# Performance work log

Hardware: AMD Instinct MI355X
Metric: run time of the kernel (lower is better)

## Reference

```python
import jax, jax.numpy as jnp
import numpy as np

B, S, H = 2, 2048, 1024
NQ, NKV, HD, RANK = 16, 4, 64, 8
THETA = 10000.0
LORA_SCALE = 16 / RANK  # alpha / rank = 2.0
ATTN_SCALE = 1.0 / np.sqrt(HD)


def setup_inputs() -> dict:
    key = jax.random.key(0)
    ks = jax.random.split(key, 14)
    n = lambda k, shape, s: jax.random.normal(k, shape, jnp.float32) * s
    return {
        "x": n(ks[0], (B, S, H), 1.0),
        # nn.Linear weights: [out_features, in_features], y = x @ W.T (scaled small for stability)
        "Wq": n(ks[1], (NQ * HD, H), 0.02),
        "Wk": n(ks[2], (NKV * HD, H), 0.02),
        "Wv": n(ks[3], (NKV * HD, H), 0.02),
        "Wo": n(ks[4], (H, NQ * HD), 0.02),
        "qA": n(ks[5], (RANK, H), 0.05), "qB": n(ks[6], (NQ * HD, RANK), 0.05),
        "kA": n(ks[7], (RANK, H), 0.05), "kB": n(ks[8], (NKV * HD, RANK), 0.05),
        "vA": n(ks[9], (RANK, H), 0.05), "vB": n(ks[10], (NKV * HD, RANK), 0.05),
        "oA": n(ks[11], (RANK, NQ * HD), 0.05), "oB": n(ks[12], (H, RANK), 0.05),
    }


def _lora_proj(x, W, A, Bm):
    # x @ W.T + ((x @ A.T) @ B.T) * lora_scaling
    return x @ W.T + ((x @ A.T) @ Bm.T) * LORA_SCALE


def _rope(x, cos_h, sin_h):
    # x: [b, h, s, d]; even/odd interleaved split, concatenated output (matches torch ref)
    x1, x2 = x[..., ::2], x[..., 1::2]
    return jnp.concatenate([x1 * cos_h - x2 * sin_h, x1 * sin_h + x2 * cos_h], axis=-1)


def _forward(x, Wq, Wk, Wv, Wo, qA, qB, kA, kB, vA, vB, oA, oB):
    b, s, _ = x.shape
    q = _lora_proj(x, Wq, qA, qB).reshape(b, s, NQ, HD).transpose(0, 2, 1, 3)
    k = _lora_proj(x, Wk, kA, kB).reshape(b, s, NKV, HD).transpose(0, 2, 1, 3)
    v = _lora_proj(x, Wv, vA, vB).reshape(b, s, NKV, HD).transpose(0, 2, 1, 3)

    inv_freq = 1.0 / (THETA ** (jnp.arange(0, HD, 2, dtype=jnp.float32) / HD))  # [HD/2]
    freqs = jnp.arange(s, dtype=jnp.float32)[:, None] * inv_freq[None, :]  # [s, HD/2]
    cos_h = jnp.cos(freqs)[None, None]  # [1,1,s,HD/2]
    sin_h = jnp.sin(freqs)[None, None]
    q = _rope(q, cos_h, sin_h)
    k = _rope(k, cos_h, sin_h)

    rep = NQ // NKV  # GQA: repeat_interleave along head axis
    k = jnp.repeat(k, rep, axis=1)
    v = jnp.repeat(v, rep, axis=1)

    attn = jax.nn.softmax(jnp.einsum('bhqd,bhkd->bhqk', q, k) * ATTN_SCALE, axis=-1)
    out = jnp.einsum('bhqk,bhkd->bhqd', attn, v)
    out = out.transpose(0, 2, 1, 3).reshape(b, s, NQ * HD)
    return _lora_proj(out, Wo, oA, oB)


def reference(x, Wq, Wk, Wv, Wo, qA, qB, kA, kB, vA, vB, oA, oB):
    return _forward(x, Wq, Wk, Wv, Wo, qA, qB, kA, kB, vA, vB, oA, oB)
```

## Files before the change

### kernel.cpp

```cpp
#include <hip/hip_runtime.h>

typedef _Float16 f16;
typedef __attribute__((ext_vector_type(8))) _Float16 f16x8;
typedef __attribute__((ext_vector_type(4))) float f32x4;

#define DI __device__ __forceinline__
#define MFMA16(a, b, c) __builtin_amdgcn_mfma_f32_16x16x32_f16(a, b, c, 0, 0, 0)

constexpr int BB = 2, SS = 2048, HH = 1024;
constexpr int NQ = 16, NKV = 4, HD = 64;
constexpr int NTOK = BB * SS;
constexpr int NQKV = NQ*HD + 2*NKV*HD;

DI f32x4 zero4() { f32x4 z = {0.f, 0.f, 0.f, 0.f}; return z; }

DI float fexp2(float x) {
#if __has_builtin(__builtin_amdgcn_exp2f)
  return __builtin_amdgcn_exp2f(x);
#else
  return exp2f(x);
#endif
}

DI unsigned pk2(float a, float b) {
#if __has_builtin(__builtin_amdgcn_cvt_pkrtz)
  typedef __fp16 fp16v2 __attribute__((ext_vector_type(2)));
  union { fp16v2 h; unsigned u; } c;
  c.h = __builtin_amdgcn_cvt_pkrtz(a, b);
  return c.u;
#else
  union { f16 h[2]; unsigned u; } c;
  c.h[0] = (f16)a; c.h[1] = (f16)b; return c.u;
#endif
}

DI void glds16(const void* g, void* l) {
  __builtin_amdgcn_global_load_lds((const __attribute__((address_space(1))) void*)g,
                                   (__attribute__((address_space(3))) void*)l, 16, 0, 0);
}

DI int shuf32(int i) {
  return (i & ~31) | (((i >> 2) & 3) << 3) | (i & 3) | (((i >> 4) & 1) << 2);
}

__global__ __launch_bounds__(256) void prep_kernel(
    const float* __restrict__ x,
    const float* __restrict__ Wq, const float* __restrict__ Wk,
    const float* __restrict__ Wv, const float* __restrict__ Wo,
    const float* __restrict__ qA, const float* __restrict__ qB,
    const float* __restrict__ kA, const float* __restrict__ kB,
    const float* __restrict__ vA, const float* __restrict__ vB,
    const float* __restrict__ oA, const float* __restrict__ oB,
    f16* __restrict__ xh, f16* __restrict__ Wqkv, f16* __restrict__ Woe,
    float* __restrict__ ctab, float* __restrict__ stab) {
  int idx = blockIdx.x * 256 + threadIdx.x;
  if (idx < NQKV * HH) {
    int n = idx >> 10, hcol = idx & 1023;
    const float *Am, *Bm; float wv; int nn;
    if (n < 1024)      { nn = n;        wv = Wq[idx];              Am = qA; Bm = qB; }
    else if (n < 1280) { nn = n - 1024; wv = Wk[nn*1024 + hcol];   Am = kA; Bm = kB; }
    else               { nn = n - 1280; wv = Wv[nn*1024 + hcol];   Am = vA; Bm = vB; }
    float s = 0.f;
#pragma unroll
    for (int r = 0; r < 8; ++r) s += Bm[nn*8 + r] * Am[r*1024 + hcol];
    Wqkv[shuf32(idx)] = (f16)(wv + 2.0f * s);
  } else if ((idx -= NQKV * HH) < 1024 * 1024) {
    int n = idx >> 10, hcol = idx & 1023;
    float s = 0.f;
#pragma unroll
    for (int r = 0; r < 8; ++r) s += oB[n*8 + r] * oA[r*1024 + hcol];
    Woe[shuf32(idx)] = (f16)(Wo[idx] + 2.0f * s);
  } else if ((idx -= 1024 * 1024) < NTOK * HH) {
    xh[shuf32(idx)] = (f16)x[idx];
  } else if ((idx -= NTOK * HH) < SS * 32) {
    int s = idx >> 5, d = idx & 31;
    float inv = expf(-(float)d * 0.28782313662425583f);
    float ang = (float)s * inv;
    ctab[idx] = cosf(ang);
    stab[idx] = sinf(ang);
  }
}

template<typename OUT_T>
__global__ __launch_bounds__(256, 2) void gemm_bt(const f16* __restrict__ A, const f16* __restrict__ Bw,
                                                  OUT_T* __restrict__ C, int M, int N, int K) {
  __shared__ char lds[65536];
  const int nt = N >> 7;
  const int nwg = (M >> 7) * nt;
  int bid = blockIdx.x;
  const int cpx = nwg >> 3;
  bid = (bid & 7) * cpx + (bid >> 3);
  const int m0 = (bid / nt) << 7;
  const int n0 = (bid % nt) << 7;
  const int tid = threadIdx.x;
  const int lane = tid & 63;
  const int w = tid >> 6, wr = w >> 1, wc = w & 1;
  const int l15 = lane & 15, g = (lane >> 4) & 3;
  const char* Ab = (const char*)A;
  const char* Bb = (const char*)Bw;
  const size_t Kb = (size_t)K * 2;
  const int srow = tid >> 3;
  const int scol = (tid & 7) << 4;

  auto stage = [&](int kt, int bs) {
    char* ab = lds + bs * 32768;
    char* bbuf = ab + 16384;
    const size_t kbyte = (size_t)kt << 7;
#pragma unroll
    for (int s = 0; s < 4; ++s) {
      int row = (s << 5) + srow;
      glds16(Ab + (size_t)(m0 + row) * Kb + kbyte + (scol ^ ((row & 7) << 4)),
             ab + (s << 12) + (w << 10));
    }
#pragma unroll
    for (int s = 0; s < 4; ++s) {
      int row = (s << 5) + srow;
      glds16(Bb + (size_t)(n0 + row) * Kb + kbyte + (scol ^ ((row & 7) << 4)),
             bbuf + (s << 12) + (w << 10));
    }
  };

  f32x4 acc[4][4];
#pragma unroll
  for (int i = 0; i < 4; ++i)
#pragma unroll
    for (int j = 0; j < 4; ++j) acc[i][j] = zero4();

  const int nkt = K >> 6;
  stage(0, 0);
  for (int t = 0; t < nkt; ++t) {
    __syncthreads();
    if (t + 1 < nkt) stage(t + 1, (t + 1) & 1);
    const char* ab = lds + (t & 1) * 32768;
    const char* bbuf = ab + 16384;
    f16x8 af[4][2], bf[4][2];
#pragma unroll
    for (int mi = 0; mi < 4; ++mi) {
      int ra = (wr << 6) + (mi << 4) + l15;
      int base = ra << 7, sw = (ra & 7) << 4;
#pragma unroll
      for (int kk = 0; kk < 2; ++kk)
        af[mi][kk] = *reinterpret_cast<const f16x8*>(ab + base + ((((kk << 6) + (g << 4))) ^ sw));
    }
#pragma unroll
    for (int nj = 0; nj < 4; ++nj) {
      int rb = (wc << 6) + (nj << 4) + l15;
      int base = rb << 7, sw = (rb & 7) << 4;
#pragma unroll
      for (int kk = 0; kk < 2; ++kk)
        bf[nj][kk] = *reinterpret_cast<const f16x8*>(bbuf + base + ((((kk << 6) + (g << 4))) ^ sw));
    }
#pragma unroll
    for (int mi = 0; mi < 4; ++mi)
#pragma unroll
      for (int nj = 0; nj < 4; ++nj) {
        acc[mi][nj] = MFMA16(af[mi][0], bf[nj][0], acc[mi][nj]);
        acc[mi][nj] = MFMA16(af[mi][1], bf[nj][1], acc[mi][nj]);
      }
  }
#pragma unroll
  for (int mi = 0; mi < 4; ++mi)
#pragma unroll
    for (int nj = 0; nj < 4; ++nj) {
      int mmb = m0 + (wr << 6) + (mi << 4) + (g << 2);
      int nn  = n0 + (wc << 6) + (nj << 4) + l15;
      f32x4 a = acc[mi][nj];
#pragma unroll
      for (int r = 0; r < 4; ++r) C[(size_t)(mmb + r) * N + nn] = (OUT_T)a[r];
    }
}

__global__ __launch_bounds__(256) void rope_kernel(const f16* __restrict__ qkv,
    const float* __restrict__ ctab, const float* __restrict__ stab,
    f16* __restrict__ Qr, f16* __restrict__ Kr) {
  int idx = blockIdx.x * 256 + threadIdx.x;
  int dp = idx & 31;
  int t = idx >> 5;
  int hh = t % 20;
  int tok = t / 20;
  int s = tok & (SS - 1), b = tok >> 11;
  float c  = ctab[(s << 5) + dp];
  float sn = stab[(s << 5) + dp];
  const f16* row = qkv + (size_t)tok * NQKV;
  int p1 = (((dp >> 2) & 3) << 3) | (dp & 3) | (((dp >> 4) & 1) << 2);
  if (hh < 16) {
    float x1 = (float)row[hh*64 + 2*dp], x2 = (float)row[hh*64 + 2*dp + 1];
    f16* out = Qr + ((size_t)(b*NQ + hh)*SS + s) * HD;
    constexpr float QS = 0.18033688011112042f;
    out[p1]      = (f16)(QS * (x1*c  - x2*sn));
    out[p1 + 32] = (f16)(QS * (x1*sn + x2*c));
  } else {
    int hk = hh - 16;
    float x1 = (float)row[1024 + hk*64 + 2*dp], x2 = (float)row[1024 + hk*64 + 2*dp + 1];
    f16* out = Kr + ((size_t)(b*NKV + hk)*SS + s) * HD;
    out[p1]      = (f16)(x1*c  - x2*sn);
    out[p1 + 32] = (f16)(x1*sn + x2*c);
  }
}

__global__ __launch_bounds__(256) void vtrans_kernel(const f16* __restrict__ qkv,
                                                     f16* __restrict__ Vt) {
  __shared__ f16 Ls[64 * 72];
  const int tid = threadIdx.x;
  const int blk = blockIdx.x;
  const int st = blk & 31, hkv = (blk >> 5) & 3, b = blk >> 7;
  const int s0 = st << 6;
  {
    int s = tid >> 2, d0 = (tid & 3) << 4;
    const f16* src = qkv + ((size_t)(b*SS + s0 + s)) * NQKV + 1280 + hkv*64 + d0;
    uint4 v0 = *reinterpret_cast<const uint4*>(src);
    uint4 v1 = *reinterpret_cast<const uint4*>(src + 8);
    *reinterpret_cast<uint4*>(Ls + s * 72 + d0) = v0;
    *reinterpret_cast<uint4*>(Ls + s * 72 + d0 + 8) = v1;
  }
  __syncthreads();
  int d = tid >> 2;
  f16* dst = Vt + ((size_t)(b*NKV + hkv)*64 + d) * SS + s0;
#pragma unroll
  for (int cc = 0; cc < 2; ++cc) {
    int cch = ((tid & 3) << 1) + cc;
    int m = cch >> 2, g = cch & 3;
    union { f16 h[8]; uint4 u; } o;
#pragma unroll
    for (int j = 0; j < 8; ++j) {
      int sl = (m << 5) + (g << 2) + (j & 3) + ((j >> 2) << 4);
      o.h[j] = Ls[sl * 72 + d];
    }
    *reinterpret_cast<uint4*>(dst + (cch << 3)) = o.u;
  }
}

__global__ __launch_bounds__(512, 4) void attn_kernel(
    const f16* __restrict__ Qr, const f16* __restrict__ Kr,
    const f16* __restrict__ Vt, f16* __restrict__ AO) {
  __shared__ char lds[3 * 16384];
  const int tid = threadIdx.x, lane = tid & 63, w = tid >> 6;
  const int l15 = lane & 15, g = (lane >> 4) & 3;
  const int bh = blockIdx.x;
  const int b = bh >> 4, h = bh & 15, hkv = h >> 2;
  const int q0 = blockIdx.y << 8;
  const char* Kbase = (const char*)(Kr + (size_t)(b*NKV + hkv) * SS * HD);
  const char* Vbase = (const char*)(Vt + (size_t)(b*NKV + hkv) * HD * SS);

  f16x8 qf[2][2];
  {
    const f16* qr0 = Qr + ((size_t)(b*NQ + h)*SS + q0 + (w << 5) + l15) * HD + (g << 3);
    qf[0][0] = *reinterpret_cast<const f16x8*>(qr0);
    qf[0][1] = *reinterpret_cast<const f16x8*>(qr0 + 32);
    qf[1][0] = *reinterpret_cast<const f16x8*>(qr0 + 16*HD);
    qf[1][1] = *reinterpret_cast<const f16x8*>(qr0 + 16*HD + 32);
  }
  f16x8 ones;
#pragma unroll
  for (int i = 0; i < 8; ++i) ones[i] = (f16)1.0f;
  const f32x4 minit = {-4.f, -4.f, -4.f, -4.f};

  f32x4 acc[4][2];
#pragma unroll
  for (int i = 0; i < 4; ++i) { acc[i][0] = zero4(); acc[i][1] = zero4(); }
  f32x4 es0 = zero4(), es1 = zero4();

  const int srow = tid >> 3;
  const int scolb = (tid & 7) << 4;
  auto stage = [&](int kv0, int buf) {
    char* kb = lds + buf * 16384;
    char* vb = kb + 8192;
    glds16(Kbase + (size_t)(kv0 + srow) * 128 + (scolb ^ ((srow & 7) << 4)),
           kb + (w << 10));
    glds16(Vbase + (size_t)srow * 4096 + (kv0 << 1) + (scolb ^ ((srow & 7) << 4)),
           vb + (w << 10));
  };

  stage(0, 0);
  stage(64, 1);
  int cur = 0;

  for (int t = 0; t < 32; ++t) {
    if (t < 31) asm volatile("s_waitcnt vmcnt(2)" ::: "memory");
    else        asm volatile("s_waitcnt vmcnt(0)" ::: "memory");
    __builtin_amdgcn_s_barrier();
    __builtin_amdgcn_sched_barrier(0);
    int nb = cur + 2; if (nb >= 3) nb -= 3;
    if (t + 2 < 32) stage((t + 2) << 6, nb);

    const char* kb = lds + cur * 16384;
    const char* vb = kb + 8192;

    f32x4 sf0[4], sf1[4];
    __builtin_amdgcn_s_setprio(1);
#pragma unroll
    for (int mb = 0; mb < 4; ++mb) {
      int rowK = (mb << 4) + l15;
      int Bk = (rowK << 7) + ((g << 4) ^ ((rowK & 7) << 4));
      f16x8 kf0 = *reinterpret_cast<const f16x8*>(kb + Bk);
      f16x8 kf1 = *reinterpret_cast<const f16x8*>(kb + (Bk ^ 64));
      f32x4 z0 = minit, z1 = minit;
      z0 = MFMA16(kf0, qf[0][0], z0); z0 = MFMA16(kf1, qf[0][1], z0);
      z1 = MFMA16(kf0, qf[1][0], z1); z1 = MFMA16(kf1, qf[1][1], z1);
      sf0[mb] = z0; sf1[mb] = z1;
    }
    __builtin_amdgcn_s_setprio(0);

    union { unsigned u[8]; f16x8 v[2]; } p0, p1;
#pragma unroll
    for (int j = 0; j < 8; ++j) {
      int mb = j >> 1, r0 = (j & 1) << 1;
      p0.u[j] = pk2(fexp2(sf0[mb][r0]), fexp2(sf0[mb][r0 + 1]));
      p1.u[j] = pk2(fexp2(sf1[mb][r0]), fexp2(sf1[mb][r0 + 1]));
    }

    __builtin_amdgcn_s_setprio(1);
#pragma unroll
    for (int sh = 0; sh < 2; ++sh) {
#pragma unroll
      for (int db = 0; db < 4; ++db) {
        int rowV = (db << 4) + l15;
        int Bv = (rowV << 7) + ((g << 4) ^ ((rowV & 7) << 4));
        f16x8 vf = *reinterpret_cast<const f16x8*>(vb + (Bv ^ (sh << 6)));
        acc[db][0] = MFMA16(vf, p0.v[sh], acc[db][0]);
        acc[db][1] = MFMA16(vf, p1.v[sh], acc[db][1]);
      }
      es0 = MFMA16(ones, p0.v[sh], es0);
      es1 = MFMA16(ones, p1.v[sh], es1);
    }
    __builtin_amdgcn_s_setprio(0);

    cur += 1; if (cur == 3) cur = 0;
  }

  float i0 = 1.0f / es0[0], i1 = 1.0f / es1[0];
  int sg0 = q0 + (w << 5) + l15;
  size_t ob0 = ((size_t)b * SS + sg0) * 1024 + h * 64;
  size_t ob1 = ob0 + (size_t)16 * 1024;
#pragma unroll
  for (int db = 0; db < 4; ++db) {
    union { f16 hv[4]; uint2 u; } o0, o1;
#pragma unroll
    for (int r = 0; r < 4; ++r) {
      o0.hv[r] = (f16)(acc[db][0][r] * i0);
      o1.hv[r] = (f16)(acc[db][1][r] * i1);
    }
    int pos = ((db >> 1) << 5) + (g << 3) + ((db & 1) << 2);
    *reinterpret_cast<uint2*>(AO + ob0 + pos) = o0.u;
    *reinterpret_cast<uint2*>(AO + ob1 + pos) = o1.u;
  }
}

extern "C" void kernel_launch(void* const* d_in, const int* in_sizes, int n_in,
                              void* d_out, int out_size, void* d_ws, size_t ws_size,
                              hipStream_t stream) {
  const float* x  = (const float*)d_in[0];
  const float* Wq = (const float*)d_in[1];
  const float* Wk = (const float*)d_in[2];
  const float* Wv = (const float*)d_in[3];
  const float* Wo = (const float*)d_in[4];
  const float* qA = (const float*)d_in[5];
  const float* qB = (const float*)d_in[6];
  const float* kA = (const float*)d_in[7];
  const float* kB = (const float*)d_in[8];
  const float* vA = (const float*)d_in[9];
  const float* vB = (const float*)d_in[10];
  const float* oA = (const float*)d_in[11];
  const float* oB = (const float*)d_in[12];
  char* ws = (char*)d_ws;
  f16* xh    = (f16*)(ws);
  f16* Wqkv  = (f16*)(ws + 8388608);
  f16* Woe   = (f16*)(ws + 11534336);
  f16* qkv   = (f16*)(ws + 13631488);
  f16* Qr    = (f16*)(ws + 26214400);
  f16* Kr    = (f16*)(ws + 34603008);
  f16* Vt    = (f16*)(ws + 36700160);
  float* ctab = (float*)(ws + 38797312);
  float* stab = (float*)(ws + 39059456);
  f16* AO = xh;
  float* out = (float*)d_out;

  prep_kernel<<<26880, 256, 0, stream>>>(x, Wq, Wk, Wv, Wo, qA, qB, kA, kB, vA, vB, oA, oB,
                                         xh, Wqkv, Woe, ctab, stab);
  gemm_bt<f16><<<dim3(32 * 12), 256, 0, stream>>>(xh, Wqkv, qkv, 4096, 1536, 1024);
  rope_kernel<<<10240, 256, 0, stream>>>(qkv, ctab, stab, Qr, Kr);
  vtrans_kernel<<<256, 256, 0, stream>>>(qkv, Vt);
  attn_kernel<<<dim3(32, 8), 512, 0, stream>>>(Qr, Kr, Vt, AO);
  gemm_bt<float><<<dim3(32 * 8), 256, 0, stream>>>(AO, Woe, out, 4096, 1024, 1024);
}
```

Before: 93.96 us.

## Split attention over two KV halves and add a combine kernel

The attention kernel now launches a third grid dimension of two splits, each covering half of the key/value sequence. Each split writes unnormalized f16 accumulators plus its row sums to workspace, and a new combine kernel adds the two partials and normalizes them. Because the softmax uses a fixed offset rather than a running max, the partials can simply be summed. The aim is to double the number of attention blocks so more of the GPU's compute units are busy; the cost is an extra launch, more memory traffic for the partials, and a risk of f16 overflow or precision loss in the unnormalized accumulators.

```diff
diff --git a/kernel.cpp b/kernel.cpp
--- a/kernel.cpp
+++ b/kernel.cpp
@@ -232,13 +232,16 @@
 
 __global__ __launch_bounds__(512, 4) void attn_kernel(
     const f16* __restrict__ Qr, const f16* __restrict__ Kr,
-    const f16* __restrict__ Vt, f16* __restrict__ AO) {
+    const f16* __restrict__ Vt, f16* __restrict__ pacc0,
+    f16* __restrict__ pacc1, float* __restrict__ pes) {
   __shared__ char lds[3 * 16384];
   const int tid = threadIdx.x, lane = tid & 63, w = tid >> 6;
   const int l15 = lane & 15, g = (lane >> 4) & 3;
   const int bh = blockIdx.x;
   const int b = bh >> 4, h = bh & 15, hkv = h >> 2;
   const int q0 = blockIdx.y << 8;
+  const int split = blockIdx.z;
+  const int kvbase = split << 10;
   const char* Kbase = (const char*)(Kr + (size_t)(b*NKV + hkv) * SS * HD);
   const char* Vbase = (const char*)(Vt + (size_t)(b*NKV + hkv) * HD * SS);
 
@@ -271,17 +274,18 @@
            vb + (w << 10));
   };
 
-  stage(0, 0);
-  stage(64, 1);
+  constexpr int NT = 16;
+  stage(kvbase, 0);
+  stage(kvbase + 64, 1);
   int cur = 0;
 
-  for (int t = 0; t < 32; ++t) {
-    if (t < 31) asm volatile("s_waitcnt vmcnt(2)" ::: "memory");
-    else        asm volatile("s_waitcnt vmcnt(0)" ::: "memory");
+  for (int t = 0; t < NT; ++t) {
+    if (t < NT - 1) asm volatile("s_waitcnt vmcnt(2)" ::: "memory");
+    else            asm volatile("s_waitcnt vmcnt(0)" ::: "memory");
     __builtin_amdgcn_s_barrier();
     __builtin_amdgcn_sched_barrier(0);
     int nb = cur + 2; if (nb >= 3) nb -= 3;
-    if (t + 2 < 32) stage((t + 2) << 6, nb);
+    if (t + 2 < NT) stage(kvbase + ((t + 2) << 6), nb);
 
     const char* kb = lds + cur * 16384;
     const char* vb = kb + 8192;
@@ -328,7 +332,7 @@
     cur += 1; if (cur == 3) cur = 0;
   }
 
-  float i0 = 1.0f / es0[0], i1 = 1.0f / es1[0];
+  f16* pout = split ? pacc1 : pacc0;
   int sg0 = q0 + (w << 5) + l15;
   size_t ob0 = ((size_t)b * SS + sg0) * 1024 + h * 64;
   size_t ob1 = ob0 + (size_t)16 * 1024;
@@ -337,13 +341,40 @@
     union { f16 hv[4]; uint2 u; } o0, o1;
 #pragma unroll
     for (int r = 0; r < 4; ++r) {
-      o0.hv[r] = (f16)(acc[db][0][r] * i0);
-      o1.hv[r] = (f16)(acc[db][1][r] * i1);
+      o0.hv[r] = (f16)acc[db][0][r];
+      o1.hv[r] = (f16)acc[db][1][r];
     }
     int pos = ((db >> 1) << 5) + (g << 3) + ((db & 1) << 2);
-    *reinterpret_cast<uint2*>(AO + ob0 + pos) = o0.u;
-    *reinterpret_cast<uint2*>(AO + ob1 + pos) = o1.u;
-  }
+    *reinterpret_cast<uint2*>(pout + ob0 + pos) = o0.u;
+    *reinterpret_cast<uint2*>(pout + ob1 + pos) = o1.u;
+  }
+  if (lane < 16) {
+    int qv = q0 + (w << 5) + lane;
+    float* pe = pes + ((size_t)(split*BB + b)*NQ + h)*SS;
+    pe[qv] = es0[0];
+    pe[qv + 16] = es1[0];
+  }
+}
+
+__global__ __launch_bounds__(256) void combine_kernel(
+    const f16* __restrict__ pacc0, const f16* __restrict__ pacc1,
+    const float* __restrict__ pes, f16* __restrict__ AO) {
+  int idx = blockIdx.x * 256 + threadIdx.x;
+  int e = idx << 3;
+  int tok = e >> 10;
+  int col = e & 1023;
+  int h = col >> 6;
+  int b = tok >> 11, q = tok & (SS - 1);
+  float e0 = pes[((size_t)(b)*NQ + h)*SS + q];
+  float e1 = pes[((size_t)(BB + b)*NQ + h)*SS + q];
+  float inv = 1.0f / (e0 + e1);
+  union { uint4 u; f16 h8[8]; } a, c, o;
+  a.u = *reinterpret_cast<const uint4*>(pacc0 + e);
+  c.u = *reinterpret_cast<const uint4*>(pacc1 + e);
+#pragma unroll
+  for (int j = 0; j < 8; ++j)
+    o.h8[j] = (f16)(((float)a.h8[j] + (float)c.h8[j]) * inv);
+  *reinterpret_cast<uint4*>(AO + e) = o.u;
 }
 
 extern "C" void kernel_launch(void* const* d_in, const int* in_sizes, int n_in,
@@ -372,7 +403,10 @@
   f16* Vt    = (f16*)(ws + 36700160);
   float* ctab = (float*)(ws + 38797312);
   float* stab = (float*)(ws + 39059456);
-  f16* AO = xh;
+  f16* pacc0 = xh;
+  f16* pacc1 = qkv;
+  float* pes = (float*)(ws + 13631488 + 8388608);
+  f16* AO = Qr;
   float* out = (float*)d_out;
 
   prep_kernel<<<26880, 256, 0, stream>>>(x, Wq, Wk, Wv, Wo, qA, qB, kA, kB, vA, vB, oA, oB,
@@ -380,6 +414,7 @@
   gemm_bt<f16><<<dim3(32 * 12), 256, 0, stream>>>(xh, Wqkv, qkv, 4096, 1536, 1024);
   rope_kernel<<<10240, 256, 0, stream>>>(qkv, ctab, stab, Qr, Kr);
   vtrans_kernel<<<256, 256, 0, stream>>>(qkv, Vt);
-  attn_kernel<<<dim3(32, 8), 512, 0, stream>>>(Qr, Kr, Vt, AO);
+  attn_kernel<<<dim3(32, 8, 2), 512, 0, stream>>>(Qr, Kr, Vt, pacc0, pacc1, pes);
+  combine_kernel<<<2048, 256, 0, stream>>>(pacc0, pacc1, pes, AO);
   gemm_bt<float><<<dim3(32 * 8), 256, 0, stream>>>(AO, Woe, out, 4096, 1024, 1024);
 }
```

Result: slower. 99.19 us (+5.6%).
